# Kernel tuning notes

Measured on AMD Instinct MI355X. Metric: run time of the kernel, lower is better.

## Reference

```python
import jax, jax.numpy as jnp
import numpy as np
from jax import lax

B, C, T = 8, 512, 2048
TEMP = 0.07
EPS = 1e-12


def setup_inputs() -> dict:
    key = jax.random.key(0)
    k1, k2, k3, k4 = jax.random.split(key, 4)
    x = jax.random.normal(k1, (B, C, T), dtype=jnp.float32)
    w_qkv = jax.random.normal(k2, (3 * C, C, 1), dtype=jnp.float32) * (1.0 / np.sqrt(C))
    w_dw = jax.random.normal(k3, (3 * C, 1, 3), dtype=jnp.float32) * (1.0 / np.sqrt(3))
    w_proj = jax.random.normal(k4, (C, C, 1), dtype=jnp.float32) * (1.0 / np.sqrt(C))
    return {"x": x, "w_qkv": w_qkv, "w_dw": w_dw, "w_proj": w_proj}


def _l2norm_ch(a):
    # F.normalize(a, dim=1): divide by L2 norm over channel dim, clamped at eps
    n = jnp.sqrt(jnp.sum(a * a, axis=1, keepdims=True))
    return a / jnp.maximum(n, EPS)


def reference(x, w_qkv, w_dw, w_proj):
    # 1x1 conv: [B,C,T] x [3C,C] -> [B,3C,T]
    qkv = jnp.einsum('bct,oc->bot', x, w_qkv[:, :, 0])
    # depthwise conv, kernel 3, padding 1, groups = 3C
    qkv = lax.conv_general_dilated(
        qkv, w_dw, window_strides=(1,), padding=[(1, 1)],
        dimension_numbers=('NCH', 'OIH', 'NCH'), feature_group_count=3 * C)
    q, k, v = jnp.split(qkv, 3, axis=1)  # each [B,C,T]
    q = _l2norm_ch(q)
    k = _l2norm_ch(k)
    # attn over tokens: [B,T,T]
    attn = jax.nn.softmax(jnp.einsum('bct,bcs->bts', q, k) / TEMP, axis=-1)
    out = jnp.einsum('bts,bcs->bct', attn, v)  # [B,C,T]
    return jnp.einsum('bct,oc->bot', out, w_proj[:, :, 0])
```

## Files before the change

kernel.cpp:

```cpp
#include <hip/hip_runtime.h>
#include <math.h>

static constexpr int B_ = 8, C_ = 512, T_ = 2048, C3_ = 1536;
static constexpr float INV_TEMP = 1.0f / 0.07f;

typedef __attribute__((ext_vector_type(8))) short short8;
typedef __attribute__((ext_vector_type(4))) float floatx4;

__device__ __forceinline__ float b2f(unsigned short u) {
  union { unsigned int i; float f; } v; v.i = ((unsigned int)u) << 16; return v.f;
}
__device__ __forceinline__ unsigned short f2b(float f) {
  union { float f; unsigned int i; } v; v.f = f;
  const unsigned int x = v.i;
  return (unsigned short)((x + 0x7FFFu + ((x >> 16) & 1u)) >> 16);
}
__device__ __forceinline__ void gld16(const unsigned short* g, unsigned short* l) {
  __builtin_amdgcn_global_load_lds(
      (const __attribute__((address_space(1))) void*)g,
      (__attribute__((address_space(3))) void*)l, 16, 0, 0);
}

template<bool OUT_BF16, int MODE, int MAP = 0>
__global__ __launch_bounds__(256)
void gemm_tn(const unsigned short* __restrict__ A, const unsigned short* __restrict__ B,
             void* __restrict__ Cout, int K, int lda, int ldb, int ldc,
             long long sA, long long sB, long long sC,
             const float* __restrict__ rs, const float* __restrict__ cs,
             float* __restrict__ denom, int rcStride, float scale)
{
  constexpr int NL = 4;

  int bz, m0, n0;
  if (MAP == 2) {
    const int id = blockIdx.x;
    bz = id & 7;
    const int r = id >> 3;
    m0 = (r >> 2) * 128; n0 = (r & 3) * 128;
  } else {
    bz = blockIdx.z;
    m0 = blockIdx.y * 128; n0 = blockIdx.x * 128;
  }
  A += (long long)bz * sA;
  B += (long long)bz * sB;
  if (MODE == 2) { rs += (long long)bz * rcStride; cs += (long long)bz * rcStride;
                   denom += (long long)bz * rcStride; }
  if (MODE == 3) { rs += (long long)bz * rcStride; }
  const int tid = threadIdx.x;
  const int w = tid >> 6, lane = tid & 63;
  const int wm = (w >> 1) * 64, wn = (w & 1) * 64;
  const int rl = lane & 15, qd = lane >> 4;

  __shared__ __align__(16) unsigned short As[3][128 * 32];
  __shared__ __align__(16) unsigned short Bs[3][128 * 32];

  const int sr = lane >> 2, sg = lane & 3;
  const int ml0 = 32 * w + sr, ml1 = ml0 + 16;
  const int q0 = sg ^ ((ml0 >> 1) & 3), q1 = sg ^ ((ml1 >> 1) & 3);
  const unsigned short* gA0 = A + (long long)(m0 + ml0) * lda + q0 * 8;
  const unsigned short* gA1 = A + (long long)(m0 + ml1) * lda + q1 * 8;
  const unsigned short* gB0 = B + (long long)(n0 + ml0) * ldb + q0 * 8;
  const unsigned short* gB1 = B + (long long)(n0 + ml1) * ldb + q1 * 8;

  int aoff[4], boff[4];
  #pragma unroll
  for (int i = 0; i < 4; ++i) {
    const int mr = wm + i * 16 + rl;
    aoff[i] = mr * 32 + ((qd ^ ((mr >> 1) & 3)) * 8);
    const int nr = wn + i * 16 + rl;
    boff[i] = nr * 32 + ((qd ^ ((nr >> 1) & 3)) * 8);
  }

  floatx4 acc[4][4];
  #pragma unroll
  for (int i = 0; i < 4; ++i)
    #pragma unroll
    for (int j = 0; j < 4; ++j) acc[i][j] = 0.0f;

  auto stage = [&](int t, int bf) {
    const int ko = t * 32;
    gld16(gA0 + ko, As[bf] + (32 * w) * 32);
    gld16(gA1 + ko, As[bf] + (32 * w + 16) * 32);
    gld16(gB0 + ko, Bs[bf] + (32 * w) * 32);
    gld16(gB1 + ko, Bs[bf] + (32 * w + 16) * 32);
  };
  auto compute = [&](int bf) {
    short8 fa[4], fb[4];
    #pragma unroll
    for (int i = 0; i < 4; ++i) fa[i] = *(const short8*)(As[bf] + aoff[i]);
    #pragma unroll
    for (int j = 0; j < 4; ++j) fb[j] = *(const short8*)(Bs[bf] + boff[j]);
    #pragma unroll
    for (int i = 0; i < 4; ++i)
      #pragma unroll
      for (int j = 0; j < 4; ++j)
        acc[i][j] = __builtin_amdgcn_mfma_f32_16x16x32_bf16(fa[i], fb[j], acc[i][j], 0, 0, 0);
  };

  const int niter = K >> 5;
  stage(0, 0);
  stage(1, 1);
  int buf = 0;
  for (int i = 0; i < niter - 1; ++i) {
    asm volatile("s_waitcnt vmcnt(%0)\n\ts_barrier" :: "i"(NL) : "memory");
    if (i + 2 < niter) {
      int nb = buf + 2; if (nb >= 3) nb -= 3;
      stage(i + 2, nb);
    }
    compute(buf);
    if (++buf == 3) buf = 0;
  }
  asm volatile("s_waitcnt vmcnt(0)\n\ts_barrier" ::: "memory");
  compute(buf);

  #pragma unroll
  for (int i = 0; i < 4; ++i) {
    #pragma unroll
    for (int r = 0; r < 4; ++r) {
      const int row = m0 + wm + i * 16 + qd * 4 + r;
      float rowf = 0.f;
      if (MODE == 2) rowf = rs[row] * scale;
      if (MODE == 3) rowf = 1.0f / rs[row];
      float rsum = 0.f;
      #pragma unroll
      for (int j = 0; j < 4; ++j) {
        const int col = n0 + wn + j * 16 + rl;
        float v = acc[i][j][r];
        if (MODE == 2) {
          const float s = v * rowf * cs[col];
          const unsigned short pb = f2b(__expf(s - scale));
          rsum += b2f(pb);
          ((unsigned short*)Cout)[(long long)bz * sC + (long long)row * ldc + col] = pb;
          continue;
        }
        if (MODE == 3) v *= rowf;
        const long long idx = (long long)bz * sC + (long long)row * ldc + col;
        if (OUT_BF16) ((unsigned short*)Cout)[idx] = f2b(v);
        else          ((float*)Cout)[idx] = v;
      }
      if (MODE == 2) {
        #pragma unroll
        for (int m = 1; m < 16; m <<= 1) rsum += __shfl_xor(rsum, m);
        if (rl == 0) atomicAdd(denom + row, rsum);
      }
    }
  }
}

template<bool OUT_BF16, int MODE, int MAP = 0>
__global__ __launch_bounds__(1024)
void gemm_tn1024(const unsigned short* __restrict__ A, const unsigned short* __restrict__ B,
                 void* __restrict__ Cout, int K, int lda, int ldb, int ldc,
                 long long sA, long long sB, long long sC,
                 const float* __restrict__ rs, const float* __restrict__ cs,
                 float* __restrict__ denom, int rcStride, float scale)
{
  extern __shared__ unsigned short S[];

  int bz, m0, n0;
  if (MAP == 1) {
    const int id = blockIdx.x;
    bz = id & 7;
    const int r = id >> 3;
    m0 = (r >> 3) * 256; n0 = (r & 7) * 256;
  } else {
    bz = blockIdx.z;
    m0 = blockIdx.y * 256; n0 = blockIdx.x * 256;
  }
  A += (long long)bz * sA;
  B += (long long)bz * sB;
  if (MODE == 2) { rs += (long long)bz * rcStride; cs += (long long)bz * rcStride;
                   denom += (long long)bz * rcStride; }
  if (MODE == 3) { rs += (long long)bz * rcStride; }
  const int tid = threadIdx.x;
  const int w = tid >> 6, lane = tid & 63;
  const int wm = (w >> 2) * 64, wn = (w & 3) * 64;
  const int rl = lane & 15, qd = lane >> 4;

  const int srow = w * 16 + (lane >> 2), sg = lane & 3;
  const int qa = sg ^ ((srow >> 1) & 3);
  const unsigned short* gA = A + (long long)(m0 + srow) * lda + qa * 8;
  const unsigned short* gB = B + (long long)(n0 + srow) * ldb + qa * 8;

  const int ar = wm + rl, br = wn + rl;
  const int aoff0 = ar * 32 + ((qd ^ ((ar >> 1) & 3)) * 8);
  const int boff0 = br * 32 + ((qd ^ ((br >> 1) & 3)) * 8);

  floatx4 acc[4][4];
  #pragma unroll
  for (int i = 0; i < 4; ++i)
    #pragma unroll
    for (int j = 0; j < 4; ++j) acc[i][j] = 0.0f;

  auto stage = [&](int t, int bf) {
    const int ko = t * 32;
    gld16(gA + ko, S + bf * 16384 + w * 512);
    gld16(gB + ko, S + bf * 16384 + 8192 + w * 512);
  };
  auto compute = [&](int bf) {
    short8 fa[4], fb[4];
    const unsigned short* pA = S + bf * 16384 + aoff0;
    const unsigned short* pB = S + bf * 16384 + 8192 + boff0;
    #pragma unroll
    for (int i = 0; i < 4; ++i) fa[i] = *(const short8*)(pA + i * 512);
    #pragma unroll
    for (int j = 0; j < 4; ++j) fb[j] = *(const short8*)(pB + j * 512);
    #pragma unroll
    for (int i = 0; i < 4; ++i)
      #pragma unroll
      for (int j = 0; j < 4; ++j)
        acc[i][j] = __builtin_amdgcn_mfma_f32_16x16x32_bf16(fa[i], fb[j], acc[i][j], 0, 0, 0);
  };

  const int niter = K >> 5;
  stage(0, 0);
  stage(1, 1);
  int buf = 0;
  for (int i = 0; i < niter - 1; ++i) {
    asm volatile("s_waitcnt vmcnt(2)\n\ts_barrier" ::: "memory");
    if (i + 2 < niter) {
      int nb = buf + 2; if (nb >= 3) nb -= 3;
      stage(i + 2, nb);
    }
    compute(buf);
    if (++buf == 3) buf = 0;
  }
  asm volatile("s_waitcnt vmcnt(0)\n\ts_barrier" ::: "memory");
  compute(buf);

  #pragma unroll
  for (int i = 0; i < 4; ++i) {
    #pragma unroll
    for (int r = 0; r < 4; ++r) {
      const int row = m0 + wm + i * 16 + qd * 4 + r;
      float rowf = 0.f;
      if (MODE == 2) rowf = rs[row] * scale;
      if (MODE == 3) rowf = 1.0f / rs[row];
      float rsum = 0.f;
      #pragma unroll
      for (int j = 0; j < 4; ++j) {
        const int col = n0 + wn + j * 16 + rl;
        float v = acc[i][j][r];
        if (MODE == 2) {
          const float s = v * rowf * cs[col];
          const unsigned short pb = f2b(__expf(s - scale));
          rsum += b2f(pb);
          ((unsigned short*)Cout)[(long long)bz * sC + (long long)row * ldc + col] = pb;
          continue;
        }
        if (MODE == 3) v *= rowf;
        const long long idx = (long long)bz * sC + (long long)row * ldc + col;
        if (OUT_BF16) ((unsigned short*)Cout)[idx] = f2b(v);
        else          ((float*)Cout)[idx] = v;
      }
      if (MODE == 2) {
        #pragma unroll
        for (int m = 1; m < 16; m <<= 1) rsum += __shfl_xor(rsum, m);
        if (rl == 0) atomicAdd(denom + row, rsum);
      }
    }
  }
}

__global__ __launch_bounds__(256)
void zero_f(float* __restrict__ p, int n)
{
  const int i = blockIdx.x * 256 + threadIdx.x;
  if (i < n) p[i] = 0.f;
}

__global__ __launch_bounds__(256)
void fin_inv(float* __restrict__ p, int n)
{
  const int i = blockIdx.x * 256 + threadIdx.x;
  if (i < n) p[i] = 1.f / fmaxf(sqrtf(p[i]), 1e-12f);
}

__global__ __launch_bounds__(256)
void conv_xT(const float* __restrict__ x, unsigned short* __restrict__ xT)
{
  const int b = blockIdx.z, t0 = blockIdx.x * 64, c0 = blockIdx.y * 64;
  const int tid = threadIdx.x;
  __shared__ float tile[64][65];
  const float* src = x + (long long)b * C_ * T_;
  const int cy = tid >> 2, g = tid & 3;
  const float* sp = src + (long long)(c0 + cy) * T_ + t0 + 16 * g;
  #pragma unroll
  for (int i = 0; i < 4; ++i) {
    const float4 v = *(const float4*)(sp + 4 * i);
    tile[cy][16 * g + 4 * i + 0] = v.x;
    tile[cy][16 * g + 4 * i + 1] = v.y;
    tile[cy][16 * g + 4 * i + 2] = v.z;
    tile[cy][16 * g + 4 * i + 3] = v.w;
  }
  __syncthreads();
  const int tl = tid >> 2, cg = tid & 3;
  short8 o0, o1;
  #pragma unroll
  for (int i = 0; i < 8; ++i) {
    o0[i] = (short)f2b(tile[16 * cg + i][tl]);
    o1[i] = (short)f2b(tile[16 * cg + 8 + i][tl]);
  }
  unsigned short* dst = xT + (long long)b * T_ * C_ + (long long)(t0 + tl) * C_ + c0 + 16 * cg;
  *(short8*)dst = o0;
  *(short8*)(dst + 8) = o1;
}

__global__ __launch_bounds__(256)
void conv_bf(const float* __restrict__ in, unsigned short* __restrict__ out, int n)
{
  const int i = blockIdx.x * 256 + threadIdx.x;
  if (i < n) out[i] = f2b(in[i]);
}

__global__ __launch_bounds__(256)
void dw_qkv_v2(const unsigned short* __restrict__ qkv, const float* __restrict__ wdw,
               unsigned short* __restrict__ qT, unsigned short* __restrict__ kT,
               unsigned short* __restrict__ vout,
               float* __restrict__ sq_q, float* __restrict__ sq_k)
{
  const int bz = blockIdx.z, b = bz / 3, p = bz % 3;
  const int t0 = blockIdx.x * 64, c0 = blockIdx.y * 64;
  const int tid = threadIdx.x;
  __shared__ unsigned short tin[64][80];
  __shared__ float tout[64][65];
  const int chb = b * C3_ + p * C_;

  #pragma unroll
  for (int s = 0; s < 2; ++s) {
    const int idx = tid + s * 256;
    const int cy = idx >> 3, g = idx & 7;
    *(short8*)&tin[cy][8 + 8 * g] =
        *(const short8*)(qkv + (long long)(chb + c0 + cy) * T_ + t0 + 8 * g);
  }
  if (tid < 64) {
    tin[tid][7] = (t0 > 0) ? qkv[(long long)(chb + c0 + tid) * T_ + t0 - 1]
                           : (unsigned short)0;
  } else if (tid < 128) {
    const int cy = tid - 64;
    tin[cy][72] = (t0 + 64 < T_) ? qkv[(long long)(chb + c0 + cy) * T_ + t0 + 64]
                                 : (unsigned short)0;
  }
  __syncthreads();

  const int cy = tid >> 2, tg = tid & 3;
  const float* wp = wdw + (p * C_ + c0 + cy) * 3;
  const float w0 = wp[0], w1 = wp[1], w2 = wp[2];

  if (p == 2) {
    short8 o0, o1;
    #pragma unroll
    for (int i = 0; i < 16; ++i) {
      const int j = 16 * tg + i;
      const float v = fmaf(w0, b2f(tin[cy][7 + j]),
                      fmaf(w1, b2f(tin[cy][8 + j]), w2 * b2f(tin[cy][9 + j])));
      if (i < 8) o0[i] = (short)f2b(v); else o1[i - 8] = (short)f2b(v);
    }
    unsigned short* d = vout + (long long)(b * C_ + c0 + cy) * T_ + t0 + 16 * tg;
    *(short8*)d = o0;
    *(short8*)(d + 8) = o1;
    return;
  }

  #pragma unroll
  for (int i = 0; i < 16; ++i) {
    const int j = 16 * tg + i;
    tout[j][cy] = fmaf(w0, b2f(tin[cy][7 + j]),
                  fmaf(w1, b2f(tin[cy][8 + j]), w2 * b2f(tin[cy][9 + j])));
  }
  __syncthreads();

  unsigned short* dst = (p == 0 ? qT : kT) + (long long)b * T_ * C_;
  float* sq = (p == 0 ? sq_q : sq_k) + (long long)b * T_;
  #pragma unroll
  for (int s = 0; s < 2; ++s) {
    const int idx = tid + s * 256;
    const int tl = idx >> 3, cl = idx & 7;
    short8 o;
    float ssq = 0.f;
    #pragma unroll
    for (int i = 0; i < 8; ++i) {
      const unsigned short ub = f2b(tout[tl][8 * cl + i]);
      o[i] = (short)ub;
      const float fv = b2f(ub);
      ssq = fmaf(fv, fv, ssq);
    }
    *(short8*)(dst + (long long)(t0 + tl) * C_ + c0 + 8 * cl) = o;
    #pragma unroll
    for (int m = 1; m < 8; m <<= 1) ssq += __shfl_xor(ssq, m);
    if (cl == 0) atomicAdd(sq + t0 + tl, ssq);
  }
}

extern "C" void kernel_launch(void* const* d_in, const int* in_sizes, int n_in,
                              void* d_out, int out_size, void* d_ws, size_t ws_size,
                              hipStream_t stream)
{
  const float* x      = (const float*)d_in[0];
  const float* w_qkv  = (const float*)d_in[1];
  const float* w_dw   = (const float*)d_in[2];
  const float* w_proj = (const float*)d_in[3];
  float* out = (float*)d_out;

  static int attr_done = 0;
  if (!attr_done) {
    hipFuncSetAttribute((const void*)&gemm_tn1024<true, 2, 1>,
                        hipFuncAttributeMaxDynamicSharedMemorySize, 98304);
    attr_done = 1;
  }

  char* base = (char*)d_ws;
  unsigned short* xT      = (unsigned short*)base;
  unsigned short* wqkv_bf = (unsigned short*)(base + 16777216);
  unsigned short* av_t    = (unsigned short*)base;
  char* p = base + 67108864;
  unsigned short* qT = (unsigned short*)p; p += 16777216;
  unsigned short* kT = (unsigned short*)p; p += 16777216;
  unsigned short* vb = (unsigned short*)p; p += 16777216;
  unsigned short* attn   = (unsigned short*)p;
  unsigned short* qkv_bf = (unsigned short*)p;
  p += 67108864;
  unsigned short* wproj_bf = (unsigned short*)p; p += 524288;
  float* inv_nq = (float*)p; p += 65536;
  float* inv_nk = (float*)p; p += 65536;
  float* denom  = (float*)p;

  const long long TC = (long long)T_ * C_, TT = (long long)T_ * T_;

  conv_xT<<<dim3(T_ / 64, C_ / 64, B_), 256, 0, stream>>>(x, xT);
  conv_bf<<<(C3_ * C_) / 256, 256, 0, stream>>>(w_qkv, wqkv_bf, C3_ * C_);
  conv_bf<<<(C_ * C_) / 256, 256, 0, stream>>>(w_proj, wproj_bf, C_ * C_);
  zero_f<<<(3 * B_ * T_) / 256, 256, 0, stream>>>(inv_nq, 3 * B_ * T_);

  gemm_tn<true, 0><<<dim3(16, 12, B_), 256, 0, stream>>>(
      wqkv_bf, xT, qkv_bf, C_, C_, C_, T_,
      0LL, TC, (long long)C3_ * T_, nullptr, nullptr, nullptr, 0, 1.f);

  dw_qkv_v2<<<dim3(T_ / 64, C_ / 64, B_ * 3), 256, 0, stream>>>(
      qkv_bf, w_dw, qT, kT, vb, inv_nq, inv_nk);
  fin_inv<<<(2 * B_ * T_) / 256, 256, 0, stream>>>(inv_nq, 2 * B_ * T_);

  gemm_tn1024<true, 2, 1><<<dim3(64 * B_, 1, 1), 1024, 98304, stream>>>(
      qT, kT, attn, C_, C_, C_, T_,
      TC, TC, TT, inv_nq, inv_nk, denom, T_, INV_TEMP);

  gemm_tn<true, 3, 2><<<dim3(64 * B_, 1, 1), 256, 0, stream>>>(
      attn, vb, av_t, T_, T_, T_, C_,
      TT, (long long)C_ * T_, TC, denom, nullptr, nullptr, T_, 1.f);

  gemm_tn<false, 0><<<dim3(16, 4, B_), 256, 0, stream>>>(
      wproj_bf, av_t, out, C_, C_, C_, T_,
      0LL, TC, (long long)C_ * T_, nullptr, nullptr, nullptr, 0, 1.f);
}
```

Before: 284.6 us.

## Make QK^T kernel persistent over two column tiles with mid-loop epilogue

Result: faster. 277.6 us (-2.5%).

```diff
diff --git a/kernel.cpp b/kernel.cpp
--- a/kernel.cpp
+++ b/kernel.cpp
@@ -147,31 +147,25 @@
   }
 }
 
-template<bool OUT_BF16, int MODE, int MAP = 0>
+template<bool OUT_BF16, int MODE>
 __global__ __launch_bounds__(1024)
-void gemm_tn1024(const unsigned short* __restrict__ A, const unsigned short* __restrict__ B,
-                 void* __restrict__ Cout, int K, int lda, int ldb, int ldc,
-                 long long sA, long long sB, long long sC,
-                 const float* __restrict__ rs, const float* __restrict__ cs,
-                 float* __restrict__ denom, int rcStride, float scale)
+void gemm_tn1024p(const unsigned short* __restrict__ A, const unsigned short* __restrict__ B,
+                  void* __restrict__ Cout, int K, int lda, int ldb, int ldc,
+                  long long sA, long long sB, long long sC,
+                  const float* __restrict__ rs, const float* __restrict__ cs,
+                  float* __restrict__ denom, int rcStride, float scale)
 {
   extern __shared__ unsigned short S[];
 
-  int bz, m0, n0;
-  if (MAP == 1) {
-    const int id = blockIdx.x;
-    bz = id & 7;
-    const int r = id >> 3;
-    m0 = (r >> 3) * 256; n0 = (r & 7) * 256;
-  } else {
-    bz = blockIdx.z;
-    m0 = blockIdx.y * 256; n0 = blockIdx.x * 256;
-  }
+  const int id = blockIdx.x;
+  const int bz = id & 7;
+  const int rr = id >> 3;
+  const int m0 = (rr >> 2) * 256;
+  const int nb = (rr & 3) * 512;
   A += (long long)bz * sA;
   B += (long long)bz * sB;
   if (MODE == 2) { rs += (long long)bz * rcStride; cs += (long long)bz * rcStride;
                    denom += (long long)bz * rcStride; }
-  if (MODE == 3) { rs += (long long)bz * rcStride; }
   const int tid = threadIdx.x;
   const int w = tid >> 6, lane = tid & 63;
   const int wm = (w >> 2) * 64, wn = (w & 3) * 64;
@@ -179,8 +173,9 @@
 
   const int srow = w * 16 + (lane >> 2), sg = lane & 3;
   const int qa = sg ^ ((srow >> 1) & 3);
-  const unsigned short* gA = A + (long long)(m0 + srow) * lda + qa * 8;
-  const unsigned short* gB = B + (long long)(n0 + srow) * ldb + qa * 8;
+  const unsigned short* gA  = A + (long long)(m0 + srow) * lda + qa * 8;
+  const unsigned short* gB0 = B + (long long)(nb + srow) * ldb + qa * 8;
+  const unsigned short* gB1 = gB0 + (long long)256 * ldb;
 
   const int ar = wm + rl, br = wn + rl;
   const int aoff0 = ar * 32 + ((qd ^ ((ar >> 1) & 3)) * 8);
@@ -193,9 +188,10 @@
     for (int j = 0; j < 4; ++j) acc[i][j] = 0.0f;
 
   auto stage = [&](int t, int bf) {
-    const int ko = t * 32;
+    const int ko = (t & 15) * 32;
+    const unsigned short* gb = (t < 16) ? gB0 : gB1;
     gld16(gA + ko, S + bf * 16384 + w * 512);
-    gld16(gB + ko, S + bf * 16384 + 8192 + w * 512);
+    gld16(gb + ko, S + bf * 16384 + 8192 + w * 512);
   };
   auto compute = [&](int bf) {
     short8 fa[4], fb[4];
@@ -211,55 +207,49 @@
       for (int j = 0; j < 4; ++j)
         acc[i][j] = __builtin_amdgcn_mfma_f32_16x16x32_bf16(fa[i], fb[j], acc[i][j], 0, 0, 0);
   };
-
-  const int niter = K >> 5;
-  stage(0, 0);
-  stage(1, 1);
-  int buf = 0;
-  for (int i = 0; i < niter - 1; ++i) {
-    asm volatile("s_waitcnt vmcnt(2)\n\ts_barrier" ::: "memory");
-    if (i + 2 < niter) {
-      int nb = buf + 2; if (nb >= 3) nb -= 3;
-      stage(i + 2, nb);
-    }
-    compute(buf);
-    if (++buf == 3) buf = 0;
-  }
-  asm volatile("s_waitcnt vmcnt(0)\n\ts_barrier" ::: "memory");
-  compute(buf);
-
-  #pragma unroll
-  for (int i = 0; i < 4; ++i) {
-    #pragma unroll
-    for (int r = 0; r < 4; ++r) {
-      const int row = m0 + wm + i * 16 + qd * 4 + r;
-      float rowf = 0.f;
-      if (MODE == 2) rowf = rs[row] * scale;
-      if (MODE == 3) rowf = 1.0f / rs[row];
-      float rsum = 0.f;
+  auto epi = [&](int n0) {
+    #pragma unroll
+    for (int i = 0; i < 4; ++i) {
       #pragma unroll
-      for (int j = 0; j < 4; ++j) {
-        const int col = n0 + wn + j * 16 + rl;
-        float v = acc[i][j][r];
-        if (MODE == 2) {
-          const float s = v * rowf * cs[col];
+      for (int r = 0; r < 4; ++r) {
+        const int row = m0 + wm + i * 16 + qd * 4 + r;
+        const float rowf = rs[row] * scale;
+        float rsum = 0.f;
+        #pragma unroll
+        for (int j = 0; j < 4; ++j) {
+          const int col = n0 + wn + j * 16 + rl;
+          const float s = acc[i][j][r] * rowf * cs[col];
           const unsigned short pb = f2b(__expf(s - scale));
           rsum += b2f(pb);
           ((unsigned short*)Cout)[(long long)bz * sC + (long long)row * ldc + col] = pb;
-          continue;
         }
-        if (MODE == 3) v *= rowf;
-        const long long idx = (long long)bz * sC + (long long)row * ldc + col;
-        if (OUT_BF16) ((unsigned short*)Cout)[idx] = f2b(v);
-        else          ((float*)Cout)[idx] = v;
-      }
-      if (MODE == 2) {
         #pragma unroll
         for (int m = 1; m < 16; m <<= 1) rsum += __shfl_xor(rsum, m);
         if (rl == 0) atomicAdd(denom + row, rsum);
       }
     }
-  }
+    #pragma unroll
+    for (int i = 0; i < 4; ++i)
+      #pragma unroll
+      for (int j = 0; j < 4; ++j) acc[i][j] = 0.0f;
+  };
+
+  stage(0, 0);
+  stage(1, 1);
+  int buf = 0;
+  for (int i = 0; i < 31; ++i) {
+    asm volatile("s_waitcnt vmcnt(2)\n\ts_barrier" ::: "memory");
+    if (i + 2 < 32) {
+      int nbuf = buf + 2; if (nbuf >= 3) nbuf -= 3;
+      stage(i + 2, nbuf);
+    }
+    compute(buf);
+    if (i == 15) epi(nb);
+    if (++buf == 3) buf = 0;
+  }
+  asm volatile("s_waitcnt vmcnt(0)\n\ts_barrier" ::: "memory");
+  compute(buf);
+  epi(nb + 256);
 }
 
 __global__ __launch_bounds__(256)
@@ -404,7 +394,7 @@
 
   static int attr_done = 0;
   if (!attr_done) {
-    hipFuncSetAttribute((const void*)&gemm_tn1024<true, 2, 1>,
+    hipFuncSetAttribute((const void*)&gemm_tn1024p<true, 2>,
                         hipFuncAttributeMaxDynamicSharedMemorySize, 98304);
     attr_done = 1;
   }
@@ -440,7 +430,7 @@
       qkv_bf, w_dw, qT, kT, vb, inv_nq, inv_nk);
   fin_inv<<<(2 * B_ * T_) / 256, 256, 0, stream>>>(inv_nq, 2 * B_ * T_);
 
-  gemm_tn1024<true, 2, 1><<<dim3(64 * B_, 1, 1), 1024, 98304, stream>>>(
+  gemm_tn1024p<true, 2><<<dim3(32 * B_, 1, 1), 1024, 98304, stream>>>(
       qT, kT, attn, C_, C_, C_, T_,
       TC, TC, TT, inv_nq, inv_nk, denom, T_, INV_TEMP);
 
```
